# Performance work log

Hardware: AMD Instinct MI355X
Metric: run time of the kernel (lower is better)

Reference implementation:

```python
import jax, jax.numpy as jnp
import numpy as np


def setup_inputs() -> dict:
    key = jax.random.key(0)
    k1, k2 = jax.random.split(key)
    B, H, W, D, C = 4, 128, 128, 128, 2
    image = jax.random.normal(k1, (B, H, W, D, C), dtype=jnp.float32)
    # near-identity affine so sampling is meaningful (localization-net output stand-in)
    theta = 0.1 * jax.random.normal(k2, (B, 3, 4), dtype=jnp.float32) + jnp.eye(3, 4, dtype=jnp.float32)[None]
    return {"image": image, "theta": theta}


def reference(image, theta):
    # Faithful port of SpatialTransformer._transform / _interpolate (incl. its
    # original index-flattening and z-weight (z1 - z0) conventions).
    B, H, W, D, C = image.shape
    oH, oW, oD = H, W, D  # downsample_factor = 1
    N = oH * oW * oD

    # _meshgrid: tf.meshgrid default 'xy' indexing -> shapes (oH, oW, oD)
    xl = jnp.linspace(-1.0, 1.0, oW)
    yl = jnp.linspace(-1.0, 1.0, oH)
    zl = jnp.linspace(-1.0, 1.0, oD)
    Xg, Yg, Zg = jnp.meshgrid(xl, yl, zl)
    grid = jnp.stack([Xg.ravel(), Yg.ravel(), Zg.ravel(), jnp.ones(N, jnp.float32)], 0)  # [4, N]

    tg = jnp.einsum('bij,jn->bin', theta.astype(jnp.float32), grid)  # [B, 3, N]
    x = tg[:, 0, :].reshape(-1)
    y = tg[:, 1, :].reshape(-1)
    z = tg[:, 2, :].reshape(-1)

    # map from [-1, 1] to pixel coords (original uses full extent, not extent-1)
    x = 0.5 * (x + 1.0) * W
    y = 0.5 * (y + 1.0) * H
    z = 0.5 * (z + 1.0) * D

    x0 = jnp.floor(x).astype(jnp.int32); x1 = x0 + 1
    y0 = jnp.floor(y).astype(jnp.int32); y1 = y0 + 1
    z0 = jnp.floor(z).astype(jnp.int32); z1 = z0 + 1
    x0 = jnp.clip(x0, 0, W - 1); x1 = jnp.clip(x1, 0, W - 1)
    y0 = jnp.clip(y0, 0, H - 1); y1 = jnp.clip(y1, 0, H - 1)
    z0 = jnp.clip(z0, 0, D - 1); z1 = jnp.clip(z1, 0, D - 1)

    base = jnp.repeat(jnp.arange(B, dtype=jnp.int32) * (H * W * D), N)  # [B*N]
    # original flat-index convention: base + y*W + z*W*H + x
    b00 = base + y0 * W + z0 * (W * H)
    b10 = base + y1 * W + z0 * (W * H)
    b01 = base + y0 * W + z1 * (W * H)
    b11 = base + y1 * W + z1 * (W * H)

    flat = image.reshape(-1, C).astype(jnp.float32)  # [B*H*W*D, C]
    pa = flat[b00 + x0]; pb = flat[b10 + x0]
    pc = flat[b00 + x1]; pd = flat[b10 + x1]
    pe = flat[b01 + x0]; pf = flat[b11 + x0]
    pg = flat[b01 + x1]; ph = flat[b11 + x1]

    x0f = x0.astype(jnp.float32); x1f = x1.astype(jnp.float32)
    y0f = y0.astype(jnp.float32); y1f = y1.astype(jnp.float32)
    z0f = z0.astype(jnp.float32); z1f = z1.astype(jnp.float32)

    wa = ((x1f - x) * (y1f - y) * (z1f - z))[:, None]
    wb = ((x1f - x) * (y - y0f) * (z1f - z))[:, None]
    wc = ((x - x0f) * (y1f - y) * (z1f - z))[:, None]
    wd = ((x - x0f) * (y - y0f) * (z1f - z))[:, None]
    we = ((x1f - x) * (y1f - y) * (z1f - z0f))[:, None]
    wf = ((x1f - x) * (y - y0f) * (z1f - z0f))[:, None]
    wg = ((x - x0f) * (y1f - y) * (z1f - z0f))[:, None]
    wh = ((x - x0f) * (y - y0f) * (z1f - z0f))[:, None]

    out = (wa * pa + wb * pb + wc * pc + wd * pd
           + we * pe + wf * pf + wg * pg + wh * ph)  # [B*N, C]
    return out.reshape(B, oH, oW, oD, C)
```

## Files before the change

### kernel.cpp

```cpp
#include <hip/hip_runtime.h>
#include <math.h>

#define BN 4
#define HN 128
#define WN 128
#define DN 128

__global__ __launch_bounds__(256) void st_trilerp_kernel(
    const float* __restrict__ image,
    const float* __restrict__ theta,
    float* __restrict__ out)
{
    const int bi = blockIdx.z;
    const int b  = bi >> 7;
    const int i  = bi & (HN - 1);
    const int j0 = blockIdx.y << 4;
    const int k0 = blockIdx.x << 4;

    const int tid = threadIdx.x;
    const int jj = tid & 15;
    const int kk = tid >> 4;
    const int j = j0 + jj;
    const int k = k0 + kk;

    const double step = 2.0 / 127.0;
    const double X = (j == WN - 1) ? 1.0 : (double)j * step - 1.0;
    const double Y = (i == HN - 1) ? 1.0 : (double)i * step - 1.0;
    const double Z = (k == DN - 1) ? 1.0 : (double)k * step - 1.0;

    const float* th = theta + b * 12;
    const double xt = (((double)th[0] * X + (double)th[1] * Y) + (double)th[2]  * Z) + (double)th[3];
    const double yt = (((double)th[4] * X + (double)th[5] * Y) + (double)th[6]  * Z) + (double)th[7];
    const double zt = (((double)th[8] * X + (double)th[9] * Y) + (double)th[10] * Z) + (double)th[11];

    const double x = (0.5 * (xt + 1.0)) * (double)WN;
    const double y = (0.5 * (yt + 1.0)) * (double)HN;
    const double z = (0.5 * (zt + 1.0)) * (double)DN;

    const int x0u = (int)floor(x);
    const int y0u = (int)floor(y);
    const int z0u = (int)floor(z);
    const int x0 = min(max(x0u,     0), WN - 1);
    const int x1 = min(max(x0u + 1, 0), WN - 1);
    const int y0 = min(max(y0u,     0), HN - 1);
    const int y1 = min(max(y0u + 1, 0), HN - 1);
    const int z0 = min(max(z0u,     0), DN - 1);
    const int z1 = min(max(z0u + 1, 0), DN - 1);

    const int base = b * (HN * WN * DN);
    const int b00 = base + y0 * WN + z0 * (WN * HN);
    const int b10 = base + y1 * WN + z0 * (WN * HN);
    const int b01 = base + y0 * WN + z1 * (WN * HN);
    const int b11 = base + y1 * WN + z1 * (WN * HN);

    const float2* __restrict__ img2 = (const float2*)image;
    const float2 pa = img2[b00 + x0];
    const float2 pb = img2[b10 + x0];
    const float2 pc = img2[b00 + x1];
    const float2 pd = img2[b10 + x1];
    const float2 pe = img2[b01 + x0];
    const float2 pf = img2[b11 + x0];
    const float2 pg = img2[b01 + x1];
    const float2 ph = img2[b11 + x1];

    const double x0f = (double)x0, x1f = (double)x1;
    const double y0f = (double)y0, y1f = (double)y1;
    const double z0f = (double)z0, z1f = (double)z1;

    const double wx0 = x1f - x, wx1 = x - x0f;
    const double wy0 = y1f - y, wy1 = y - y0f;
    const double wz0 = z1f - z, wzA = z1f - z0f;

    const float wa = (float)(wx0 * wy0 * wz0);
    const float wb = (float)(wx0 * wy1 * wz0);
    const float wc = (float)(wx1 * wy0 * wz0);
    const float wd = (float)(wx1 * wy1 * wz0);
    const float we = (float)(wx0 * wy0 * wzA);
    const float wf = (float)(wx0 * wy1 * wzA);
    const float wg = (float)(wx1 * wy0 * wzA);
    const float wh = (float)(wx1 * wy1 * wzA);

    float2 o;
    o.x = wa * pa.x + wb * pb.x + wc * pc.x + wd * pd.x
        + we * pe.x + wf * pf.x + wg * pg.x + wh * ph.x;
    o.y = wa * pa.y + wb * pb.y + wc * pc.y + wd * pd.y
        + we * pe.y + wf * pf.y + wg * pg.y + wh * ph.y;

    __shared__ float2 tile[16][17];
    tile[kk][jj] = o;
    __syncthreads();

    const int kw = tid & 15;
    const int jw = tid >> 4;
    const int oidx = (bi * WN + (j0 + jw)) * DN + (k0 + kw);
    ((float2*)out)[oidx] = tile[kw][jw];
}

extern "C" void kernel_launch(void* const* d_in, const int* in_sizes, int n_in,
                              void* d_out, int out_size, void* d_ws, size_t ws_size,
                              hipStream_t stream) {
    const float* image = (const float*)d_in[0];
    const float* theta = (const float*)d_in[1];
    float* out = (float*)d_out;

    dim3 grid(DN / 16, WN / 16, BN * HN);
    st_trilerp_kernel<<<grid, 256, 0, stream>>>(image, theta, out);
}
```

Baseline: 149.5 us.

## Merge adjacent-x corner gathers into float4 loads and compute weights in fp32

The x0 and x1 neighbours sit next to each other in memory, so each of the four y/z corner rows is now fetched with one 16-byte float4 load instead of two float2 loads. A clamped base index keeps the load in bounds, and selects pick out the right pair. The corner-weight products also move from double to float, which cuts fp64 work but may change rounding slightly. One risk is that a float4 load at an odd float2 index is only 8-byte aligned, which may split the access or need a dword-level load.

```diff
diff --git a/kernel.cpp b/kernel.cpp
--- a/kernel.cpp
+++ b/kernel.cpp
@@ -54,31 +54,38 @@
     const int b11 = base + y1 * WN + z1 * (WN * HN);
 
     const float2* __restrict__ img2 = (const float2*)image;
-    const float2 pa = img2[b00 + x0];
-    const float2 pb = img2[b10 + x0];
-    const float2 pc = img2[b00 + x1];
-    const float2 pd = img2[b10 + x1];
-    const float2 pe = img2[b01 + x0];
-    const float2 pf = img2[b11 + x0];
-    const float2 pg = img2[b01 + x1];
-    const float2 ph = img2[b11 + x1];
 
-    const double x0f = (double)x0, x1f = (double)x1;
-    const double y0f = (double)y0, y1f = (double)y1;
-    const double z0f = (double)z0, z1f = (double)z1;
+    const int xb = min(x0, WN - 2);
+    const bool lo0 = (x0 == xb);
+    const bool lo1 = (x1 == xb);
 
-    const double wx0 = x1f - x, wx1 = x - x0f;
-    const double wy0 = y1f - y, wy1 = y - y0f;
-    const double wz0 = z1f - z, wzA = z1f - z0f;
+    const float4 q00 = *(const float4*)(img2 + b00 + xb);
+    const float4 q10 = *(const float4*)(img2 + b10 + xb);
+    const float4 q01 = *(const float4*)(img2 + b01 + xb);
+    const float4 q11 = *(const float4*)(img2 + b11 + xb);
 
-    const float wa = (float)(wx0 * wy0 * wz0);
-    const float wb = (float)(wx0 * wy1 * wz0);
-    const float wc = (float)(wx1 * wy0 * wz0);
-    const float wd = (float)(wx1 * wy1 * wz0);
-    const float we = (float)(wx0 * wy0 * wzA);
-    const float wf = (float)(wx0 * wy1 * wzA);
-    const float wg = (float)(wx1 * wy0 * wzA);
-    const float wh = (float)(wx1 * wy1 * wzA);
+    const float2 pa = lo0 ? make_float2(q00.x, q00.y) : make_float2(q00.z, q00.w);
+    const float2 pc = lo1 ? make_float2(q00.x, q00.y) : make_float2(q00.z, q00.w);
+    const float2 pb = lo0 ? make_float2(q10.x, q10.y) : make_float2(q10.z, q10.w);
+    const float2 pd = lo1 ? make_float2(q10.x, q10.y) : make_float2(q10.z, q10.w);
+    const float2 pe = lo0 ? make_float2(q01.x, q01.y) : make_float2(q01.z, q01.w);
+    const float2 pg = lo1 ? make_float2(q01.x, q01.y) : make_float2(q01.z, q01.w);
+    const float2 pf = lo0 ? make_float2(q11.x, q11.y) : make_float2(q11.z, q11.w);
+    const float2 ph = lo1 ? make_float2(q11.x, q11.y) : make_float2(q11.z, q11.w);
+
+    const float wx0 = (float)((double)x1 - x), wx1 = (float)(x - (double)x0);
+    const float wy0 = (float)((double)y1 - y), wy1 = (float)(y - (double)y0);
+    const float wz0 = (float)((double)z1 - z);
+    const float wzA = (float)(z1 - z0);
+
+    const float wa = wx0 * wy0 * wz0;
+    const float wb = wx0 * wy1 * wz0;
+    const float wc = wx1 * wy0 * wz0;
+    const float wd = wx1 * wy1 * wz0;
+    const float we = wx0 * wy0 * wzA;
+    const float wf = wx0 * wy1 * wzA;
+    const float wg = wx1 * wy0 * wzA;
+    const float wh = wx1 * wy1 * wzA;
 
     float2 o;
     o.x = wa * pa.x + wb * pb.x + wc * pc.x + wd * pd.x
```

New measurement: 145.1 us. 2.9% less time.
